# Kernel optimization log

Hardware: AMD Instinct MI355X
Metric: run time of the kernel (lower is better)

## Reference

```python
import jax, jax.numpy as jnp
import numpy as np

B, P, C = 32, 8732, 21
TOP_K = 200
CONF_THRESH = 0.01
NMS_THRESH = 0.45
VAR0, VAR1 = 0.1, 0.2  # VOC PRIOR_BOX VARIANCE


def setup_inputs() -> dict:
    key = jax.random.key(0)
    k1, k2, k3 = jax.random.split(key, 3)
    loc_data = jax.random.normal(k1, (B, P, 4), jnp.float32)
    conf_data = jax.random.uniform(k2, (B, P, C), jnp.float32)
    prior_data = jax.random.uniform(k3, (P, 4), jnp.float32)
    return {"loc_data": loc_data, "conf_data": conf_data, "prior_data": prior_data}


def _decode(loc, priors):
    # priors are (cx, cy, w, h); returns (x1, y1, x2, y2)
    cxcy = priors[:, :2] + loc[:, :2] * VAR0 * priors[:, 2:]
    wh = priors[:, 2:] * jnp.exp(loc[:, 2:] * VAR1)
    x1y1 = cxcy - wh * 0.5
    return jnp.concatenate([x1y1, x1y1 + wh], axis=1)  # [P,4]


def _nms_class(boxes, scores):
    # boxes [P,4], scores [P] -> [TOP_K,5] rows of (score, x1, y1, x2, y2)
    s = jnp.where(scores > CONF_THRESH, scores, -1.0)
    top_s, idx = jax.lax.top_k(s, TOP_K)          # descending scores
    b = boxes[idx]                                 # [K,4]
    valid = top_s > CONF_THRESH
    x1, y1, x2, y2 = b[:, 0], b[:, 1], b[:, 2], b[:, 3]
    area = (x2 - x1) * (y2 - y1)
    # pairwise intersection / IoU [K,K]
    xx1 = jnp.maximum(x1[:, None], x1[None, :])
    yy1 = jnp.maximum(y1[:, None], y1[None, :])
    xx2 = jnp.minimum(x2[:, None], x2[None, :])
    yy2 = jnp.minimum(y2[:, None], y2[None, :])
    inter = jnp.clip(xx2 - xx1, 0.0) * jnp.clip(yy2 - yy1, 0.0)
    union = area[:, None] + area[None, :] - inter
    iou = inter / union
    ar = jnp.arange(TOP_K)

    def step(carry, j):
        kept, suppressed = carry
        is_kept = valid[j] & ~suppressed[j]
        kept = kept.at[j].set(is_kept)
        suppressed = suppressed | (is_kept & (iou[j] > NMS_THRESH) & (ar > j))
        return (kept, suppressed), None

    (kept, _), _ = jax.lax.scan(
        step, (jnp.zeros(TOP_K, bool), jnp.zeros(TOP_K, bool)), ar)
    # compact kept rows to the front (matches output[i, cl, :count] = ...)
    pos = jnp.cumsum(kept) - 1
    safe = jnp.where(kept, pos, TOP_K)
    rows = jnp.concatenate([top_s[:, None], b], axis=1)  # [K,5]
    out = jnp.zeros((TOP_K + 1, 5), rows.dtype).at[safe].set(rows)[:TOP_K]
    return out


def reference(loc_data, conf_data, prior_data):
    def per_image(loc, conf):
        boxes = _decode(loc, prior_data)           # [P,4]
        return jax.vmap(lambda s: _nms_class(boxes, s), in_axes=1)(conf)  # [C,K,5]

    out = jax.vmap(per_image)(loc_data, conf_data)  # [B,C,K,5]
    return out.at[:, 0].set(0.0)  # class 0 (background) is skipped in original
```

## Files before the change

kernel.cpp:

```cpp
#include <hip/hip_runtime.h>
#include <stdint.h>

#define B_ 32
#define P_ 8732
#define C_ 21
#define TOPK 200
#define TGT 228
#define TGT0 300
#define SUBCAP 28
#define NCH2 35
#define NSLOT (NCH2 * SUBCAP)
#define CONF_T 0.01f
#define NMS_T 0.45f
#define NT 512
#define KV4 5
#define NTASK (B_ * C_)

__device__ __forceinline__ uint32_t f2s(float f) {
    uint32_t u = __float_as_uint(f);
    return (u & 0x80000000u) ? ~u : (u | 0x80000000u);
}
__device__ __forceinline__ float s2f(uint32_t s) {
    uint32_t b = (s & 0x80000000u) ? (s & 0x7FFFFFFFu) : ~s;
    return __uint_as_float(b);
}
__device__ __forceinline__ uint32_t keyof(float v) {
    return f2s((v > CONF_T) ? v : -1.0f);
}
__device__ __forceinline__ uint32_t thr0() {
    return f2s(1.0f - (float)TGT0 / (float)P_);
}

__global__ __launch_bounds__(256) void scatter_cands(const float* __restrict__ conf,
                                                     uint32_t* __restrict__ gccnt,
                                                     uint64_t* __restrict__ gcand) {
    const int b = blockIdx.x / NCH2;
    const int ch = blockIdx.x % NCH2;
    const int p0 = ch * 256;
    const int n = min(256, P_ - p0);
    const int tid = threadIdx.x;
    const int lane = tid & 63;
    const int cs = tid >> 6;
    __shared__ float tile[256 * C_];
    const float4* src4 = (const float4*)(conf + ((size_t)b * P_ + p0) * C_);
    float4* tile4 = (float4*)tile;
    const int tot4 = (n * C_) >> 2;
    for (int i = tid; i < tot4; i += 256) tile4[i] = src4[i];
    __syncthreads();
    const uint32_t T0 = thr0();
    for (int c = (cs == 0 ? 4 : cs); c < C_; c += 4) {
        uint32_t kk[4];
        #pragma unroll
        for (int k = 0; k < 4; ++k) {
            const int r = lane + 64 * k;
            if (r < n) kk[k] = keyof(tile[r * C_ + c]);
            else       kk[k] = 0u;
        }
        const unsigned long long m0 = __ballot(kk[0] >= T0);
        const unsigned long long m1 = __ballot(kk[1] >= T0);
        const unsigned long long m2 = __ballot(kk[2] >= T0);
        const unsigned long long m3 = __ballot(kk[3] >= T0);
        const int c0 = __popcll(m0), c1 = __popcll(m1), c2 = __popcll(m2), c3 = __popcll(m3);
        const int total = c0 + c1 + c2 + c3;
        const int task = b * C_ + c;
        uint64_t* dst = gcand + ((size_t)task * NCH2 + ch) * SUBCAP;
        {
            const unsigned long long below = (1ull << lane) - 1ull;
            const int cum[4] = {0, c0, c0 + c1, c0 + c1 + c2};
            const unsigned long long mm[4] = {m0, m1, m2, m3};
            #pragma unroll
            for (int k = 0; k < 4; ++k) {
                if (kk[k] >= T0) {
                    const int pos = cum[k] + __popcll(mm[k] & below);
                    if (pos < SUBCAP) {
                        const int p = p0 + lane + 64 * k;
                        dst[pos] = ((uint64_t)kk[k] << 32) | (uint32_t)(~(uint32_t)p);
                    }
                }
            }
        }
        if (lane == 0) gccnt[(size_t)task * NCH2 + ch] = (uint32_t)total;
    }
}

template<bool HASWS>
__global__ __launch_bounds__(NT, 6) void detect_kernel(
    const float* __restrict__ loc, const float* __restrict__ prior,
    const uint32_t* __restrict__ gccnt, const uint64_t* __restrict__ gcand,
    const float* __restrict__ conf, float* __restrict__ out)
{
    const int task = blockIdx.x;
    const int b = task / C_;
    const int c = task % C_;
    const int tid = threadIdx.x;
    const int lane = tid & 63;
    float* outp = out + (size_t)task * TOPK * 5;

    if (c == 0) {
        for (int e = tid; e < TOPK * 5; e += NT) outp[e] = 0.0f;
        return;
    }

    __shared__ uint64_t cand[256];
    __shared__ float4 bbox[TOPK];
    __shared__ float bs[TOPK];
    __shared__ float sar[TOPK];
    __shared__ unsigned long long msk[TOPK * 4];
    __shared__ unsigned long long vmask[4];
    __shared__ int order[TOPK];
    __shared__ int s_cnt, s_nk;
    __shared__ int s_c2[2];
    __shared__ int s_c3[3];
    __shared__ uint32_t s_ccnt[NCH2];
    __shared__ int s_gc, s_bad;

    const uint32_t T0 = thr0();

    if (tid == 0) s_cnt = 0;
    if (tid < 2) s_c2[tid] = 0;
    if (tid < 3) s_c3[tid] = 0;
    if (HASWS && tid < NCH2) s_ccnt[tid] = gccnt[(size_t)task * NCH2 + tid];
    for (int i2 = tid; i2 < TOPK * 4; i2 += NT) msk[i2] = 0ull;
    __syncthreads();
    if (HASWS && tid < 64) {
        uint32_t cc = (lane < NCH2) ? s_ccnt[lane] : 0u;
        int bad = (cc > SUBCAP) ? 1 : 0;
        int tot = (int)cc;
        #pragma unroll
        for (int d = 1; d < 64; d <<= 1) {
            tot += __shfl_down(tot, d);
            bad |= __shfl_down(bad, d);
        }
        if (lane == 0) { s_gc = tot; s_bad = bad; }
    }
    __syncthreads();

    const bool fast = HASWS && !s_bad && s_gc >= TOPK;
    const int gc = HASWS ? s_gc : 0;

    uint64_t vc0 = 0, vc1 = 0;
    bool val0 = false, val1 = false;
    uint4 kv[KV4];
    if (fast) {
        const uint64_t* gp = gcand + (size_t)task * NSLOT;
        {
            const int ch0 = tid / SUBCAP, i0 = tid - ch0 * SUBCAP;
            if (i0 < (int)s_ccnt[ch0]) { vc0 = gp[tid]; val0 = true; }
        }
        const int s1 = tid + NT;
        if (s1 < NSLOT) {
            const int ch1 = s1 / SUBCAP, i1 = s1 - ch1 * SUBCAP;
            if (i1 < (int)s_ccnt[ch1]) { vc1 = gp[s1]; val1 = true; }
        }
    } else {
        const float* sp = conf + (size_t)b * P_ * C_ + c;
        #pragma unroll
        for (int r = 0; r < KV4; ++r) {
            uint32_t uu[4];
            #pragma unroll
            for (int c4 = 0; c4 < 4; ++c4) {
                int p = (tid + r * NT) * 4 + c4;
                if (p < P_) {
                    float v = sp[(size_t)p * C_];
                    v = (v > CONF_T) ? v : -1.0f;
                    uu[c4] = f2s(v);
                } else uu[c4] = 0u;
            }
            kv[r] = make_uint4(uu[0], uu[1], uu[2], uu[3]);
        }
    }

    if (fast) {
        const uint32_t k0 = (uint32_t)(vc0 >> 32);
        const uint32_t k1 = (uint32_t)(vc1 >> 32);
        uint32_t vthr = T0;
        if (gc > 256) {
            uint32_t lo = T0, hi = 0xFFFFFFFFu;
            uint32_t t;
            {
                const float sc = s2f(T0);
                const float sn = 1.0f - (1.0f - sc) * (float)TGT / (float)gc;
                t = f2s(sn);
                if (!(t > lo && t < hi)) t = lo + ((hi - lo) >> 1);
            }
            for (int it = 0; ; ++it) {
                const int slot = it % 3;
                int my = (val0 && k0 >= t) + (val1 && k1 >= t);
                #pragma unroll
                for (int d = 1; d < 64; d <<= 1) my += __shfl_down(my, d);
                if (lane == 0) atomicAdd(&s_c3[slot], my);
                if (tid == 0) s_c3[(it + 1) % 3] = 0;
                __syncthreads();
                const int cnt = s_c3[slot];
                if (cnt >= TOPK && cnt <= 256) { vthr = t; break; }
                if (cnt > 256) lo = t; else hi = t;
                if (hi - lo <= 1) { vthr = lo; break; }
                uint32_t tn = 0;
                bool bis = (it >= 8) || (cnt == 0);
                if (!bis) {
                    const float sc = s2f(t);
                    const float sn = 1.0f - (1.0f - sc) * (float)TGT / (float)cnt;
                    tn = f2s(sn);
                    if (!(tn > lo && tn < hi)) bis = true;
                }
                if (bis) tn = lo + ((hi - lo) >> 1);
                t = tn;
            }
        }
        const bool p0v = val0 && k0 >= vthr;
        const bool p1v = val1 && k1 >= vthr;
        const unsigned long long mm0 = __ballot(p0v);
        const unsigned long long mm1 = __ballot(p1v);
        const int wtot = __popcll(mm0) + __popcll(mm1);
        int base = 0;
        if (lane == 0 && wtot) base = atomicAdd(&s_cnt, wtot);
        base = __shfl(base, 0);
        const unsigned long long below = (1ull << lane) - 1ull;
        const int o0 = base + __popcll(mm0 & below);
        const int o1 = base + __popcll(mm0) + __popcll(mm1 & below);
        if (p0v && o0 < 256) cand[o0] = vc0;
        if (p1v && o1 < 256) cand[o1] = vc1;
    } else {
        uint32_t lo = 0u, hi = 0xFFFFFFFFu;
        uint32_t t = f2s(1.0f - (float)TGT / (float)P_);
        uint32_t vthr = 0u;
        for (int it = 0; ; ++it) {
            const int slot = it & 1;
            int my = 0;
            #pragma unroll
            for (int r = 0; r < KV4; ++r)
                my += (kv[r].x >= t) + (kv[r].y >= t) + (kv[r].z >= t) + (kv[r].w >= t);
            #pragma unroll
            for (int d = 1; d < 64; d <<= 1) my += __shfl_down(my, d);
            if (lane == 0) atomicAdd(&s_c2[slot], my);
            __syncthreads();
            const int cnt = s_c2[slot];
            __syncthreads();
            if (tid == 0) s_c2[slot] = 0;
            if (cnt >= TOPK && cnt <= 256) { vthr = t; break; }
            if (cnt > 256) lo = t; else hi = t;
            if (hi - lo <= 1) { vthr = lo; break; }
            uint32_t tn = 0;
            bool bis = (it >= 8) || (cnt == 0);
            if (!bis) {
                const float sc = s2f(t);
                const float sn = 1.0f - (1.0f - sc) * (float)TGT / (float)cnt;
                tn = f2s(sn);
                if (!(tn > lo && tn < hi)) bis = true;
            }
            if (bis) tn = lo + ((hi - lo) >> 1);
            t = tn;
        }
        #pragma unroll
        for (int r = 0; r < KV4; ++r) {
            const int pb = (tid + r * NT) * 4;
            uint32_t uu[4] = {kv[r].x, kv[r].y, kv[r].z, kv[r].w};
            #pragma unroll
            for (int c4 = 0; c4 < 4; ++c4) {
                uint32_t u = uu[c4];
                if (u >= vthr) {
                    int pos = atomicAdd(&s_cnt, 1);
                    if (pos < 256) cand[pos] = ((uint64_t)u << 32) | (uint32_t)(~(uint32_t)(pb + c4));
                }
            }
        }
    }
    __syncthreads();
    if (tid < 256 && tid >= s_cnt) cand[tid] = 0ull;
    __syncthreads();

    uint64_t v = (tid < 256) ? cand[tid] : 0ull;
    for (int kk = 2; kk <= 256; kk <<= 1) {
        for (int j = kk >> 1; j > 0; j >>= 1) {
            if (j >= 64) {
                __syncthreads();
                if (tid < 256) cand[tid] = v;
                __syncthreads();
                if (tid < 256) {
                    uint64_t pv = cand[tid ^ j];
                    bool keepmax = (((tid & j) == 0) == ((tid & kk) == 0));
                    v = keepmax ? (v > pv ? v : pv) : (v < pv ? v : pv);
                }
            } else if (tid < 256) {
                uint64_t pv = __shfl_xor(v, j);
                bool keepmax = (((tid & j) == 0) == ((tid & kk) == 0));
                v = keepmax ? (v > pv ? v : pv) : (v < pv ? v : pv);
            }
        }
    }

    float my_sc = -1.0f;
    if (tid < TOPK) {
        uint32_t su = (uint32_t)(v >> 32);
        int p = (int)(~(uint32_t)v);
        my_sc = s2f(su);
        const float4 l4 = *(const float4*)(loc + ((size_t)b * P_ + p) * 4);
        const float4 pr = *(const float4*)(prior + (size_t)p * 4);
        float cx = __fadd_rn(pr.x, __fmul_rn(__fmul_rn(l4.x, 0.1f), pr.z));
        float cy = __fadd_rn(pr.y, __fmul_rn(__fmul_rn(l4.y, 0.1f), pr.w));
        float ew = (float)exp((double)__fmul_rn(l4.z, 0.2f));
        float eh = (float)exp((double)__fmul_rn(l4.w, 0.2f));
        float w  = __fmul_rn(pr.z, ew);
        float h  = __fmul_rn(pr.w, eh);
        float x1 = __fsub_rn(cx, __fmul_rn(w, 0.5f));
        float y1 = __fsub_rn(cy, __fmul_rn(h, 0.5f));
        float x2 = __fadd_rn(x1, w);
        float y2 = __fadd_rn(y1, h);
        bs[tid] = my_sc;
        bbox[tid] = make_float4(x1, y1, x2, y2);
        sar[tid] = __fmul_rn(__fsub_rn(x2, x1), __fsub_rn(y2, y1));
    }
    {
        unsigned long long bm = __ballot(tid < TOPK && my_sc > CONF_T);
        if (lane == 0 && tid < 256) vmask[tid >> 6] = bm;
    }
    __syncthreads();

    if (tid < 500) {
        const int rp = tid / 5;
        const int s  = tid - rp * 5;
        #pragma unroll
        for (int pass = 0; pass < 2; ++pass) {
            const int j  = pass ? (199 - rp) : rp;
            const int i0 = j + 1 + s;
            const float4 bj = bbox[j];
            const float  aj = sar[j];
            unsigned long long* mrow = &msk[j * 4];
            auto iou1 = [&](int i) {
                const float4 bi = bbox[i];
                float xx1 = fmaxf(bj.x, bi.x);
                float yy1 = fmaxf(bj.y, bi.y);
                float xx2 = fminf(bj.z, bi.z);
                float yy2 = fminf(bj.w, bi.w);
                float dx = fmaxf(__fsub_rn(xx2, xx1), 0.0f);
                float dy = fmaxf(__fsub_rn(yy2, yy1), 0.0f);
                float inter = __fmul_rn(dx, dy);
                if (inter > 0.0f) {
                    float ai = sar[i];
                    float uni = __fsub_rn(__fadd_rn(aj, ai), inter);
                    float t45 = __fmul_rn(NMS_T, uni);
                    float mar = __fmul_rn(t45, 1e-6f);
                    bool sup;
                    if (inter > __fadd_rn(t45, mar)) sup = true;
                    else if (inter < __fsub_rn(t45, mar)) sup = false;
                    else sup = (inter / uni > NMS_T);
                    if (sup) atomicOr(&mrow[i >> 6], 1ull << (i & 63));
                }
            };
            int i = i0;
            for (; i + 5 < TOPK; i += 10) { iou1(i); iou1(i + 5); }
            if (i < TOPK) iou1(i);
        }
    }
    __syncthreads();

    if (tid < 64) {
        const int L = tid;
        auto or_reduce = [&](unsigned long long x) {
            #pragma unroll
            for (int d = 1; d < 64; d <<= 1) x |= __shfl_xor(x, d);
            return x;
        };
        unsigned long long s1 = 0, s2 = 0, s3 = 0;
        int nk = 0;
        #pragma unroll
        for (int w = 0; w < 4; ++w) {
            const int j = (w << 6) | L;
            unsigned long long r0 = 0, r1 = 0, r2 = 0, r3 = 0;
            if (j < TOPK) {
                const unsigned long long* mr = &msk[j * 4];
                r0 = mr[0]; r1 = mr[1]; r2 = mr[2]; r3 = mr[3];
            }
            const unsigned long long rself = (w == 0) ? r0 : (w == 1) ? r1
                                           : (w == 2) ? r2 : r3;
            unsigned long long sw = (w == 0) ? 0ull : (w == 1) ? s1
                                  : (w == 2) ? s2 : s3;
            unsigned long long alive = vmask[w] & ~sw;
            unsigned long long pm = 0;
            while (alive) {
                int jl = __ffsll(alive) - 1;
                if (L == 0) order[nk] = (w << 6) | jl;
                ++nk;
                sw |= __shfl(rself, jl);
                pm |= (1ull << jl);
                alive &= ~(sw | (1ull << jl));
            }
            if (pm) {
                const bool picked = (pm >> L) & 1ull;
                if (w == 0) {
                    s1 |= or_reduce(picked ? r1 : 0ull);
                    s2 |= or_reduce(picked ? r2 : 0ull);
                    s3 |= or_reduce(picked ? r3 : 0ull);
                } else if (w == 1) {
                    s2 |= or_reduce(picked ? r2 : 0ull);
                    s3 |= or_reduce(picked ? r3 : 0ull);
                } else if (w == 2) {
                    s3 |= or_reduce(picked ? r3 : 0ull);
                }
            }
        }
        if (L == 0) s_nk = nk;
    }
    __syncthreads();

    const int nk = s_nk;
    for (int e = tid; e < TOPK * 5; e += NT) {
        int r = e / 5;
        int f = e - r * 5;
        float val = 0.0f;
        if (r < nk) {
            int j = order[r];
            float4 bb = bbox[j];
            val = (f == 0) ? bs[j] : (f == 1) ? bb.x : (f == 2) ? bb.y
                : (f == 3) ? bb.z : bb.w;
        }
        outp[e] = val;
    }
}

extern "C" void kernel_launch(void* const* d_in, const int* in_sizes, int n_in,
                              void* d_out, int out_size, void* d_ws, size_t ws_size,
                              hipStream_t stream) {
    const float* loc   = (const float*)d_in[0];
    const float* conf  = (const float*)d_in[1];
    const float* prior = (const float*)d_in[2];
    float* out = (float*)d_out;

    const size_t cnt_bytes  = (size_t)NTASK * NCH2 * sizeof(uint32_t);
    const size_t cand_bytes = (size_t)NTASK * NSLOT * sizeof(uint64_t);
    if (ws_size >= cnt_bytes + cand_bytes) {
        uint32_t* gccnt = (uint32_t*)d_ws;
        uint64_t* gcand = (uint64_t*)((char*)d_ws + cnt_bytes);
        scatter_cands<<<B_ * NCH2, 256, 0, stream>>>(conf, gccnt, gcand);
        detect_kernel<true><<<NTASK, NT, 0, stream>>>(loc, prior, gccnt, gcand, conf, out);
    } else {
        detect_kernel<false><<<NTASK, NT, 0, stream>>>(loc, prior, nullptr, nullptr, conf, out);
    }
}
```

Before: 122.6 us.

## Sort all precomputed candidates directly with 512-wide bitonic, decode before sorting

The fast path drops the iterative threshold search that cut candidates down to 256. Instead it compacts all workspace candidates, up to 512, into shared memory with a prefix-sum offset per chunk, and sorts them with a 512-wide bitonic sort using ping-pong buffers. Box decoding now runs for every candidate before the sort, and the sort key carries a slot index so the top 200 rows just copy the decoded box. This removes the barrier-heavy threshold loop, but it doubles the sort width, decodes more boxes (with double-precision exp), and adds shared-memory arrays that may lower occupancy.

```diff
diff --git a/kernel.cpp b/kernel.cpp
--- a/kernel.cpp
+++ b/kernel.cpp
@@ -10,6 +10,7 @@
 #define SUBCAP 28
 #define NCH2 35
 #define NSLOT (NCH2 * SUBCAP)
+#define SORTN 512
 #define CONF_T 0.01f
 #define NMS_T 0.45f
 #define NT 512
@@ -101,7 +102,10 @@
         return;
     }
 
-    __shared__ uint64_t cand[256];
+    __shared__ uint64_t cA[SORTN];
+    __shared__ uint64_t cB[SORTN];
+    __shared__ float4 bbox512[SORTN];
+    __shared__ float  sar512[SORTN];
     __shared__ float4 bbox[TOPK];
     __shared__ float bs[TOPK];
     __shared__ float sar[TOPK];
@@ -110,50 +114,71 @@
     __shared__ int order[TOPK];
     __shared__ int s_cnt, s_nk;
     __shared__ int s_c2[2];
-    __shared__ int s_c3[3];
     __shared__ uint32_t s_ccnt[NCH2];
+    __shared__ int s_cbase[NCH2];
     __shared__ int s_gc, s_bad;
-
-    const uint32_t T0 = thr0();
 
     if (tid == 0) s_cnt = 0;
     if (tid < 2) s_c2[tid] = 0;
-    if (tid < 3) s_c3[tid] = 0;
     if (HASWS && tid < NCH2) s_ccnt[tid] = gccnt[(size_t)task * NCH2 + tid];
+    cA[tid] = 0ull;
     for (int i2 = tid; i2 < TOPK * 4; i2 += NT) msk[i2] = 0ull;
     __syncthreads();
     if (HASWS && tid < 64) {
         uint32_t cc = (lane < NCH2) ? s_ccnt[lane] : 0u;
-        int bad = (cc > SUBCAP) ? 1 : 0;
-        int tot = (int)cc;
+        int incl = (int)cc;
         #pragma unroll
         for (int d = 1; d < 64; d <<= 1) {
-            tot += __shfl_down(tot, d);
-            bad |= __shfl_down(bad, d);
-        }
-        if (lane == 0) { s_gc = tot; s_bad = bad; }
-    }
-    __syncthreads();
-
-    const bool fast = HASWS && !s_bad && s_gc >= TOPK;
+            int t = __shfl_up(incl, d);
+            if (lane >= d) incl += t;
+        }
+        unsigned long long bb = __ballot(cc > SUBCAP);
+        if (lane < NCH2) s_cbase[lane] = incl - (int)cc;
+        if (lane == 63) { s_gc = incl; s_bad = (bb != 0ull) ? 1 : 0; }
+    }
+    __syncthreads();
+
     const int gc = HASWS ? s_gc : 0;
-
-    uint64_t vc0 = 0, vc1 = 0;
-    bool val0 = false, val1 = false;
-    uint4 kv[KV4];
+    const bool fast = HASWS && !s_bad && gc >= TOPK && gc <= SORTN;
+
+    auto decode_to = [&](uint32_t key, int p, int pos) {
+        const float4 l4 = *(const float4*)(loc + ((size_t)b * P_ + p) * 4);
+        const float4 pr = *(const float4*)(prior + (size_t)p * 4);
+        float cx = __fadd_rn(pr.x, __fmul_rn(__fmul_rn(l4.x, 0.1f), pr.z));
+        float cy = __fadd_rn(pr.y, __fmul_rn(__fmul_rn(l4.y, 0.1f), pr.w));
+        float ew = (float)exp((double)__fmul_rn(l4.z, 0.2f));
+        float eh = (float)exp((double)__fmul_rn(l4.w, 0.2f));
+        float w  = __fmul_rn(pr.z, ew);
+        float h  = __fmul_rn(pr.w, eh);
+        float x1 = __fsub_rn(cx, __fmul_rn(w, 0.5f));
+        float y1 = __fsub_rn(cy, __fmul_rn(h, 0.5f));
+        float x2 = __fadd_rn(x1, w);
+        float y2 = __fadd_rn(y1, h);
+        bbox512[pos] = make_float4(x1, y1, x2, y2);
+        sar512[pos] = __fmul_rn(__fsub_rn(x2, x1), __fsub_rn(y2, y1));
+        cA[pos] = ((uint64_t)key << 32)
+                | ((uint64_t)(0x3FFFu - (uint32_t)p) << 10)
+                | (uint32_t)pos;
+    };
+
     if (fast) {
         const uint64_t* gp = gcand + (size_t)task * NSLOT;
-        {
-            const int ch0 = tid / SUBCAP, i0 = tid - ch0 * SUBCAP;
-            if (i0 < (int)s_ccnt[ch0]) { vc0 = gp[tid]; val0 = true; }
-        }
-        const int s1 = tid + NT;
-        if (s1 < NSLOT) {
-            const int ch1 = s1 / SUBCAP, i1 = s1 - ch1 * SUBCAP;
-            if (i1 < (int)s_ccnt[ch1]) { vc1 = gp[s1]; val1 = true; }
+        #pragma unroll
+        for (int h = 0; h < 2; ++h) {
+            const int sidx = tid + h * NT;
+            if (sidx < NSLOT) {
+                const int ch = sidx / SUBCAP, i = sidx - ch * SUBCAP;
+                if (i < (int)s_ccnt[ch]) {
+                    const uint64_t vc = gp[sidx];
+                    const uint32_t key = (uint32_t)(vc >> 32);
+                    const int p = (int)(~(uint32_t)vc);
+                    decode_to(key, p, s_cbase[ch] + i);
+                }
+            }
         }
     } else {
         const float* sp = conf + (size_t)b * P_ * C_ + c;
+        uint4 kv[KV4];
         #pragma unroll
         for (int r = 0; r < KV4; ++r) {
             uint32_t uu[4];
@@ -168,59 +193,6 @@
             }
             kv[r] = make_uint4(uu[0], uu[1], uu[2], uu[3]);
         }
-    }
-
-    if (fast) {
-        const uint32_t k0 = (uint32_t)(vc0 >> 32);
-        const uint32_t k1 = (uint32_t)(vc1 >> 32);
-        uint32_t vthr = T0;
-        if (gc > 256) {
-            uint32_t lo = T0, hi = 0xFFFFFFFFu;
-            uint32_t t;
-            {
-                const float sc = s2f(T0);
-                const float sn = 1.0f - (1.0f - sc) * (float)TGT / (float)gc;
-                t = f2s(sn);
-                if (!(t > lo && t < hi)) t = lo + ((hi - lo) >> 1);
-            }
-            for (int it = 0; ; ++it) {
-                const int slot = it % 3;
-                int my = (val0 && k0 >= t) + (val1 && k1 >= t);
-                #pragma unroll
-                for (int d = 1; d < 64; d <<= 1) my += __shfl_down(my, d);
-                if (lane == 0) atomicAdd(&s_c3[slot], my);
-                if (tid == 0) s_c3[(it + 1) % 3] = 0;
-                __syncthreads();
-                const int cnt = s_c3[slot];
-                if (cnt >= TOPK && cnt <= 256) { vthr = t; break; }
-                if (cnt > 256) lo = t; else hi = t;
-                if (hi - lo <= 1) { vthr = lo; break; }
-                uint32_t tn = 0;
-                bool bis = (it >= 8) || (cnt == 0);
-                if (!bis) {
-                    const float sc = s2f(t);
-                    const float sn = 1.0f - (1.0f - sc) * (float)TGT / (float)cnt;
-                    tn = f2s(sn);
-                    if (!(tn > lo && tn < hi)) bis = true;
-                }
-                if (bis) tn = lo + ((hi - lo) >> 1);
-                t = tn;
-            }
-        }
-        const bool p0v = val0 && k0 >= vthr;
-        const bool p1v = val1 && k1 >= vthr;
-        const unsigned long long mm0 = __ballot(p0v);
-        const unsigned long long mm1 = __ballot(p1v);
-        const int wtot = __popcll(mm0) + __popcll(mm1);
-        int base = 0;
-        if (lane == 0 && wtot) base = atomicAdd(&s_cnt, wtot);
-        base = __shfl(base, 0);
-        const unsigned long long below = (1ull << lane) - 1ull;
-        const int o0 = base + __popcll(mm0 & below);
-        const int o1 = base + __popcll(mm0) + __popcll(mm1 & below);
-        if (p0v && o0 < 256) cand[o0] = vc0;
-        if (p1v && o1 < 256) cand[o1] = vc1;
-    } else {
         uint32_t lo = 0u, hi = 0xFFFFFFFFu;
         uint32_t t = f2s(1.0f - (float)TGT / (float)P_);
         uint32_t vthr = 0u;
@@ -260,30 +232,27 @@
                 uint32_t u = uu[c4];
                 if (u >= vthr) {
                     int pos = atomicAdd(&s_cnt, 1);
-                    if (pos < 256) cand[pos] = ((uint64_t)u << 32) | (uint32_t)(~(uint32_t)(pb + c4));
-                }
-            }
-        }
-    }
-    __syncthreads();
-    if (tid < 256 && tid >= s_cnt) cand[tid] = 0ull;
-    __syncthreads();
-
-    uint64_t v = (tid < 256) ? cand[tid] : 0ull;
-    for (int kk = 2; kk <= 256; kk <<= 1) {
+                    if (pos < 256) decode_to(u, pb + c4, pos);
+                }
+            }
+        }
+    }
+    __syncthreads();
+
+    uint64_t v = cA[tid];
+    int pp = 0;
+    for (int kk = 2; kk <= SORTN; kk <<= 1) {
         for (int j = kk >> 1; j > 0; j >>= 1) {
+            const bool keepmax = (((tid & j) == 0) == ((tid & kk) == 0));
             if (j >= 64) {
+                uint64_t* wb = pp ? cB : cA;
+                wb[tid] = v;
                 __syncthreads();
-                if (tid < 256) cand[tid] = v;
-                __syncthreads();
-                if (tid < 256) {
-                    uint64_t pv = cand[tid ^ j];
-                    bool keepmax = (((tid & j) == 0) == ((tid & kk) == 0));
-                    v = keepmax ? (v > pv ? v : pv) : (v < pv ? v : pv);
-                }
-            } else if (tid < 256) {
+                uint64_t pv = wb[tid ^ j];
+                pp ^= 1;
+                v = keepmax ? (v > pv ? v : pv) : (v < pv ? v : pv);
+            } else {
                 uint64_t pv = __shfl_xor(v, j);
-                bool keepmax = (((tid & j) == 0) == ((tid & kk) == 0));
                 v = keepmax ? (v > pv ? v : pv) : (v < pv ? v : pv);
             }
         }
@@ -291,24 +260,12 @@
 
     float my_sc = -1.0f;
     if (tid < TOPK) {
-        uint32_t su = (uint32_t)(v >> 32);
-        int p = (int)(~(uint32_t)v);
-        my_sc = s2f(su);
-        const float4 l4 = *(const float4*)(loc + ((size_t)b * P_ + p) * 4);
-        const float4 pr = *(const float4*)(prior + (size_t)p * 4);
-        float cx = __fadd_rn(pr.x, __fmul_rn(__fmul_rn(l4.x, 0.1f), pr.z));
-        float cy = __fadd_rn(pr.y, __fmul_rn(__fmul_rn(l4.y, 0.1f), pr.w));
-        float ew = (float)exp((double)__fmul_rn(l4.z, 0.2f));
-        float eh = (float)exp((double)__fmul_rn(l4.w, 0.2f));
-        float w  = __fmul_rn(pr.z, ew);
-        float h  = __fmul_rn(pr.w, eh);
-        float x1 = __fsub_rn(cx, __fmul_rn(w, 0.5f));
-        float y1 = __fsub_rn(cy, __fmul_rn(h, 0.5f));
-        float x2 = __fadd_rn(x1, w);
-        float y2 = __fadd_rn(y1, h);
+        const uint32_t key = (uint32_t)(v >> 32);
+        const int slot = (int)(v & 0x3FFu);
+        my_sc = s2f(key);
         bs[tid] = my_sc;
-        bbox[tid] = make_float4(x1, y1, x2, y2);
-        sar[tid] = __fmul_rn(__fsub_rn(x2, x1), __fsub_rn(y2, y1));
+        bbox[tid] = bbox512[slot];
+        sar[tid] = sar512[slot];
     }
     {
         unsigned long long bm = __ballot(tid < TOPK && my_sc > CONF_T);
```

New measurement: 124.9 us. About the same (+1.9%).

## Decode candidate boxes before sort and double-buffer bitonic shared stages

Applied to the files above, without the earlier changes.

Box decoding (loc/prior loads and exp) moves from after the bitonic sort to the moment each candidate is compacted, so the global loads can overlap the sort. The sort key now packs the score, the prior index and the slot, so the sorted order can gather precomputed boxes from shared memory. The cross-wave bitonic stages ping-pong between two shared buffers, which removes one barrier per stage. The chunk-count reduction is replaced by a per-thread serial sum, and the candidate loads are issued before the fast-path test is known. In exchange, shared memory use grows (reducing possible occupancy), up to 256 boxes are decoded instead of 200, and the packing assumes the prior index fits in 14 bits.

```diff
diff --git a/kernel.cpp b/kernel.cpp
--- a/kernel.cpp
+++ b/kernel.cpp
@@ -102,6 +102,9 @@
     }
 
     __shared__ uint64_t cand[256];
+    __shared__ uint64_t cB[256];
+    __shared__ float4 bbox256[256];
+    __shared__ float  sar256[256];
     __shared__ float4 bbox[TOPK];
     __shared__ float bs[TOPK];
     __shared__ float sar[TOPK];
@@ -112,7 +115,6 @@
     __shared__ int s_c2[2];
     __shared__ int s_c3[3];
     __shared__ uint32_t s_ccnt[NCH2];
-    __shared__ int s_gc, s_bad;
 
     const uint32_t T0 = thr0();
 
@@ -122,53 +124,57 @@
     if (HASWS && tid < NCH2) s_ccnt[tid] = gccnt[(size_t)task * NCH2 + tid];
     for (int i2 = tid; i2 < TOPK * 4; i2 += NT) msk[i2] = 0ull;
     __syncthreads();
-    if (HASWS && tid < 64) {
-        uint32_t cc = (lane < NCH2) ? s_ccnt[lane] : 0u;
-        int bad = (cc > SUBCAP) ? 1 : 0;
-        int tot = (int)cc;
-        #pragma unroll
-        for (int d = 1; d < 64; d <<= 1) {
-            tot += __shfl_down(tot, d);
-            bad |= __shfl_down(bad, d);
-        }
-        if (lane == 0) { s_gc = tot; s_bad = bad; }
-    }
-    __syncthreads();
-
-    const bool fast = HASWS && !s_bad && s_gc >= TOPK;
-    const int gc = HASWS ? s_gc : 0;
 
     uint64_t vc0 = 0, vc1 = 0;
-    bool val0 = false, val1 = false;
-    uint4 kv[KV4];
-    if (fast) {
+    int ch0 = 0, i0 = 0, ch1 = 0, i1 = 0;
+    bool inr1 = false;
+    if (HASWS) {
         const uint64_t* gp = gcand + (size_t)task * NSLOT;
-        {
-            const int ch0 = tid / SUBCAP, i0 = tid - ch0 * SUBCAP;
-            if (i0 < (int)s_ccnt[ch0]) { vc0 = gp[tid]; val0 = true; }
-        }
+        ch0 = tid / SUBCAP; i0 = tid - ch0 * SUBCAP;
+        vc0 = gp[tid];
         const int s1 = tid + NT;
         if (s1 < NSLOT) {
-            const int ch1 = s1 / SUBCAP, i1 = s1 - ch1 * SUBCAP;
-            if (i1 < (int)s_ccnt[ch1]) { vc1 = gp[s1]; val1 = true; }
-        }
-    } else {
-        const float* sp = conf + (size_t)b * P_ * C_ + c;
-        #pragma unroll
-        for (int r = 0; r < KV4; ++r) {
-            uint32_t uu[4];
-            #pragma unroll
-            for (int c4 = 0; c4 < 4; ++c4) {
-                int p = (tid + r * NT) * 4 + c4;
-                if (p < P_) {
-                    float v = sp[(size_t)p * C_];
-                    v = (v > CONF_T) ? v : -1.0f;
-                    uu[c4] = f2s(v);
-                } else uu[c4] = 0u;
-            }
-            kv[r] = make_uint4(uu[0], uu[1], uu[2], uu[3]);
-        }
-    }
+            ch1 = s1 / SUBCAP; i1 = s1 - ch1 * SUBCAP;
+            vc1 = gp[s1];
+            inr1 = true;
+        }
+    }
+
+    int gc = 0; bool bad = false;
+    if (HASWS) {
+        #pragma unroll
+        for (int k = 0; k < NCH2; ++k) {
+            const uint32_t cc = s_ccnt[k];
+            gc += (int)cc;
+            bad |= (cc > SUBCAP);
+        }
+    }
+    const bool fast = HASWS && !bad && gc >= TOPK;
+
+    const bool val0 = fast && (i0 < (int)s_ccnt[ch0]);
+    const bool val1 = fast && inr1 && (i1 < (int)s_ccnt[ch1]);
+
+    auto decode_to = [&](int p, int pos) {
+        const float4 l4 = *(const float4*)(loc + ((size_t)b * P_ + p) * 4);
+        const float4 pr = *(const float4*)(prior + (size_t)p * 4);
+        float cx = __fadd_rn(pr.x, __fmul_rn(__fmul_rn(l4.x, 0.1f), pr.z));
+        float cy = __fadd_rn(pr.y, __fmul_rn(__fmul_rn(l4.y, 0.1f), pr.w));
+        float ew = (float)exp((double)__fmul_rn(l4.z, 0.2f));
+        float eh = (float)exp((double)__fmul_rn(l4.w, 0.2f));
+        float w  = __fmul_rn(pr.z, ew);
+        float h  = __fmul_rn(pr.w, eh);
+        float x1 = __fsub_rn(cx, __fmul_rn(w, 0.5f));
+        float y1 = __fsub_rn(cy, __fmul_rn(h, 0.5f));
+        float x2 = __fadd_rn(x1, w);
+        float y2 = __fadd_rn(y1, h);
+        bbox256[pos] = make_float4(x1, y1, x2, y2);
+        sar256[pos] = __fmul_rn(__fsub_rn(x2, x1), __fsub_rn(y2, y1));
+    };
+    auto pack = [](uint32_t key, int p, int pos) -> uint64_t {
+        return ((uint64_t)key << 32)
+             | ((uint64_t)(0x3FFFu - (uint32_t)p) << 10)
+             | (uint32_t)pos;
+    };
 
     if (fast) {
         const uint32_t k0 = (uint32_t)(vc0 >> 32);
@@ -218,9 +224,33 @@
         const unsigned long long below = (1ull << lane) - 1ull;
         const int o0 = base + __popcll(mm0 & below);
         const int o1 = base + __popcll(mm0) + __popcll(mm1 & below);
-        if (p0v && o0 < 256) cand[o0] = vc0;
-        if (p1v && o1 < 256) cand[o1] = vc1;
+        if (p0v && o0 < 256) {
+            const int p = (int)(~(uint32_t)vc0);
+            cand[o0] = pack(k0, p, o0);
+            decode_to(p, o0);
+        }
+        if (p1v && o1 < 256) {
+            const int p = (int)(~(uint32_t)vc1);
+            cand[o1] = pack(k1, p, o1);
+            decode_to(p, o1);
+        }
     } else {
+        const float* sp = conf + (size_t)b * P_ * C_ + c;
+        uint4 kv[KV4];
+        #pragma unroll
+        for (int r = 0; r < KV4; ++r) {
+            uint32_t uu[4];
+            #pragma unroll
+            for (int c4 = 0; c4 < 4; ++c4) {
+                int p = (tid + r * NT) * 4 + c4;
+                if (p < P_) {
+                    float v = sp[(size_t)p * C_];
+                    v = (v > CONF_T) ? v : -1.0f;
+                    uu[c4] = f2s(v);
+                } else uu[c4] = 0u;
+            }
+            kv[r] = make_uint4(uu[0], uu[1], uu[2], uu[3]);
+        }
         uint32_t lo = 0u, hi = 0xFFFFFFFFu;
         uint32_t t = f2s(1.0f - (float)TGT / (float)P_);
         uint32_t vthr = 0u;
@@ -260,7 +290,10 @@
                 uint32_t u = uu[c4];
                 if (u >= vthr) {
                     int pos = atomicAdd(&s_cnt, 1);
-                    if (pos < 256) cand[pos] = ((uint64_t)u << 32) | (uint32_t)(~(uint32_t)(pb + c4));
+                    if (pos < 256) {
+                        cand[pos] = pack(u, pb + c4, pos);
+                        decode_to(pb + c4, pos);
+                    }
                 }
             }
         }
@@ -270,20 +303,21 @@
     __syncthreads();
 
     uint64_t v = (tid < 256) ? cand[tid] : 0ull;
+    int pp = 0;
     for (int kk = 2; kk <= 256; kk <<= 1) {
         for (int j = kk >> 1; j > 0; j >>= 1) {
+            const bool keepmax = (((tid & j) == 0) == ((tid & kk) == 0));
             if (j >= 64) {
-                __syncthreads();
-                if (tid < 256) cand[tid] = v;
+                uint64_t* wb = pp ? cB : cand;
+                if (tid < 256) wb[tid] = v;
                 __syncthreads();
                 if (tid < 256) {
-                    uint64_t pv = cand[tid ^ j];
-                    bool keepmax = (((tid & j) == 0) == ((tid & kk) == 0));
+                    uint64_t pv = wb[tid ^ j];
                     v = keepmax ? (v > pv ? v : pv) : (v < pv ? v : pv);
                 }
+                pp ^= 1;
             } else if (tid < 256) {
                 uint64_t pv = __shfl_xor(v, j);
-                bool keepmax = (((tid & j) == 0) == ((tid & kk) == 0));
                 v = keepmax ? (v > pv ? v : pv) : (v < pv ? v : pv);
             }
         }
@@ -291,24 +325,12 @@
 
     float my_sc = -1.0f;
     if (tid < TOPK) {
-        uint32_t su = (uint32_t)(v >> 32);
-        int p = (int)(~(uint32_t)v);
-        my_sc = s2f(su);
-        const float4 l4 = *(const float4*)(loc + ((size_t)b * P_ + p) * 4);
-        const float4 pr = *(const float4*)(prior + (size_t)p * 4);
-        float cx = __fadd_rn(pr.x, __fmul_rn(__fmul_rn(l4.x, 0.1f), pr.z));
-        float cy = __fadd_rn(pr.y, __fmul_rn(__fmul_rn(l4.y, 0.1f), pr.w));
-        float ew = (float)exp((double)__fmul_rn(l4.z, 0.2f));
-        float eh = (float)exp((double)__fmul_rn(l4.w, 0.2f));
-        float w  = __fmul_rn(pr.z, ew);
-        float h  = __fmul_rn(pr.w, eh);
-        float x1 = __fsub_rn(cx, __fmul_rn(w, 0.5f));
-        float y1 = __fsub_rn(cy, __fmul_rn(h, 0.5f));
-        float x2 = __fadd_rn(x1, w);
-        float y2 = __fadd_rn(y1, h);
+        const uint32_t key = (uint32_t)(v >> 32);
+        const int slot = (int)(v & 0x3FFu);
+        my_sc = s2f(key);
         bs[tid] = my_sc;
-        bbox[tid] = make_float4(x1, y1, x2, y2);
-        sar[tid] = __fmul_rn(__fsub_rn(x2, x1), __fsub_rn(y2, y1));
+        bbox[tid] = bbox256[slot];
+        sar[tid] = sar256[slot];
     }
     {
         unsigned long long bm = __ballot(tid < TOPK && my_sc > CONF_T);
@@ -322,7 +344,7 @@
         #pragma unroll
         for (int pass = 0; pass < 2; ++pass) {
             const int j  = pass ? (199 - rp) : rp;
-            const int i0 = j + 1 + s;
+            const int i0b = j + 1 + s;
             const float4 bj = bbox[j];
             const float  aj = sar[j];
             unsigned long long* mrow = &msk[j * 4];
@@ -347,7 +369,7 @@
                     if (sup) atomicOr(&mrow[i >> 6], 1ull << (i & 63));
                 }
             };
-            int i = i0;
+            int i = i0b;
             for (; i + 5 < TOPK; i += 10) { iou1(i); iou1(i + 5); }
             if (i < TOPK) iou1(i);
         }
```

Result: slower. 125.2 us (+2.1%).
